# Optimization experiments

Measured on AMD Instinct MI355X. Metric: run time of the kernel, lower is better.

## Reference

```python
import jax, jax.numpy as jnp
import numpy as np

DIM = 384
WS = 7
NH = 12
N = WS ** 3          # 343 tokens per window
BW = 256             # number of windows (batch*num_windows)
HD = DIM // NH       # head dim = 32


def _rel_pos_index(ws: int) -> np.ndarray:
    coords = np.stack(np.meshgrid(np.arange(ws), np.arange(ws), np.arange(ws), indexing='ij'))
    coords = coords.reshape(3, -1)                       # [3, N]
    rel = coords[:, :, None] - coords[:, None, :]        # [3, N, N]
    rel = rel.transpose(1, 2, 0)                         # [N, N, 3]
    rel = rel + (ws - 1)
    idx = rel[..., 0] * (2 * ws - 1) ** 2 + rel[..., 1] * (2 * ws - 1) + rel[..., 2]
    return idx.astype(np.int32)                          # [N, N]


def setup_inputs() -> dict:
    key = jax.random.key(0)
    ks = jax.random.split(key, 6)
    x = jax.random.normal(ks[0], (BW, N, DIM), dtype=jnp.float32)
    qkv_w = jax.random.normal(ks[1], (DIM, 3 * DIM), dtype=jnp.float32) * (DIM ** -0.5)
    qkv_b = jax.random.normal(ks[2], (3 * DIM,), dtype=jnp.float32) * 0.02
    proj_w = jax.random.normal(ks[3], (DIM, DIM), dtype=jnp.float32) * (DIM ** -0.5)
    proj_b = jax.random.normal(ks[4], (DIM,), dtype=jnp.float32) * 0.02
    bias_table = jax.random.normal(ks[5], ((2 * WS - 1) ** 3, NH), dtype=jnp.float32) * 0.02
    rel_pos_index = jnp.asarray(_rel_pos_index(WS))
    return {"x": x, "qkv_w": qkv_w, "qkv_b": qkv_b, "proj_w": proj_w,
            "proj_b": proj_b, "bias_table": bias_table, "rel_pos_index": rel_pos_index}


def reference(x, qkv_w, qkv_b, proj_w, proj_b, bias_table, rel_pos_index):
    B_, n, C = x.shape
    scale = (C // NH) ** -0.5
    qkv = (x @ qkv_w + qkv_b).reshape(B_, n, 3, NH, C // NH)
    q, k, v = qkv[:, :, 0], qkv[:, :, 1], qkv[:, :, 2]   # [B_, n, H, d]
    # scores: [B_, H, n, n]
    attn = jnp.einsum('bihd,bjhd->bhij', q, k) * scale
    rel_bias = bias_table[rel_pos_index]                  # [n, n, H]
    attn = attn + rel_bias.transpose(2, 0, 1)[None]
    attn = jax.nn.softmax(attn, axis=-1)
    out = jnp.einsum('bhij,bjhd->bihd', attn, v).reshape(B_, n, C)
    return out @ proj_w + proj_b
```

## Files before the change

kernel.cpp:

```cpp
#include <hip/hip_runtime.h>


#define M_TOT 87808
#define NTOK  343
#define DIMC  384
#define NHEAD 12
#define QKVN  1152
#define BWIN  256
#define TSLAB (22 * 11 * 512)

typedef __bf16 bf16x8 __attribute__((ext_vector_type(8)));
typedef __bf16 bf16x4 __attribute__((ext_vector_type(4)));
typedef float f32x4 __attribute__((ext_vector_type(4)));
typedef unsigned short u16x4 __attribute__((ext_vector_type(4)));
typedef unsigned short u16x8 __attribute__((ext_vector_type(8)));

__device__ __forceinline__ unsigned short bf16rne(float f) {
  unsigned int u = __float_as_uint(f);
  u += 0x7fffu + ((u >> 16) & 1u);
  return (unsigned short)(u >> 16);
}

__device__ __forceinline__ unsigned int packbf(float lo, float hi) {
  return (unsigned int)bf16rne(lo) | ((unsigned int)bf16rne(hi) << 16);
}

__device__ __forceinline__ bf16x4 pack_bf16x4(float a, float b, float c, float d) {
  unsigned ua = __float_as_uint(a) + 0x8000u;
  unsigned ub = __float_as_uint(b) + 0x8000u;
  unsigned uc = __float_as_uint(c) + 0x8000u;
  unsigned ud = __float_as_uint(d) + 0x8000u;
  unsigned lo = __builtin_amdgcn_perm(ub, ua, 0x07060302u);
  unsigned hi = __builtin_amdgcn_perm(ud, uc, 0x07060302u);
  union { unsigned u[2]; bf16x4 v; } x;
  x.u[0] = lo; x.u[1] = hi;
  return x.v;
}

__device__ __forceinline__ float bf16tof(unsigned short s) {
  return __uint_as_float(((unsigned int)s) << 16);
}

__device__ __forceinline__ u16x4 lo4(u16x8 v) { return __builtin_shufflevector(v, v, 0, 1, 2, 3); }
__device__ __forceinline__ u16x4 hi4(u16x8 v) { return __builtin_shufflevector(v, v, 4, 5, 6, 7); }


__global__ void cvt_x_kernel(const float* __restrict__ x, unsigned short* __restrict__ xb, int n8) {
  int i = blockIdx.x * 256 + threadIdx.x;
  if (i >= n8) return;
  const float4* xv = (const float4*)x + (size_t)i * 2;
  float4 a = xv[0], b = xv[1];
  uint4 o;
  o.x = packbf(a.x, a.y); o.y = packbf(a.z, a.w);
  o.z = packbf(b.x, b.y); o.w = packbf(b.z, b.w);
  ((uint4*)xb)[i] = o;
}

__global__ void prep_w_kernel(const float* __restrict__ qkv_w, const float* __restrict__ proj_w,
                              unsigned short* __restrict__ wqkvT, unsigned short* __restrict__ wprojT) {
  int tid = blockIdx.x * 256 + threadIdx.x;
  if (tid < QKVN * DIMC) {
    int n = tid / DIMC, k = tid - n * DIMC;
    wqkvT[tid] = bf16rne(qkv_w[(size_t)k * QKVN + n]);
  }
  if (tid < DIMC * DIMC) {
    int n = tid / DIMC, k = tid - n * DIMC;
    wprojT[tid] = bf16rne(proj_w[(size_t)k * DIMC + n]);
  }
}

__global__ void prep_biasT_kernel(const float* __restrict__ bias_table, const int* __restrict__ rel_idx,
                                  unsigned short* __restrict__ biasT) {
  int tid = blockIdx.x * 256 + threadIdx.x;
  if (tid >= NHEAD * 22 * 11 * 64) return;
  int l15 = tid & 15;
  int q   = (tid >> 4) & 3;
  int rest = tid >> 6;
  int jp  = rest % 11;
  int it  = (rest / 11) % 22;
  int h   = rest / (11 * 22);
  int i = it * 16 + l15; if (i > NTOK - 1) i = NTOK - 1;
  const float LOG2E = 1.44269504088896340f;
  u16x8 out;
  #pragma unroll
  for (int e = 0; e < 8; e++) {
    int jt = 2 * jp + (e >> 2), r = e & 3;
    int j = jt * 16 + 4 * q + r;
    float v;
    if (j < NTOK) {
      int idx = rel_idx[i * NTOK + j];
      v = bias_table[idx * NHEAD + h] * LOG2E;
    } else {
      v = -1e30f;
    }
    out[e] = bf16rne(v);
  }
  *(u16x8*)(biasT + (size_t)tid * 8) = out;
}


typedef const __attribute__((address_space(1))) unsigned int* gas_t;
typedef __attribute__((address_space(3))) unsigned int* las_t;

__device__ __forceinline__ void load16_lds(const void* g, void* l) {
  __builtin_amdgcn_global_load_lds((gas_t)g, (las_t)l, 16, 0, 0);
}

template<int OUT_MODE>
__global__ __launch_bounds__(256, 3) void gemm_bt_kernel(
    const unsigned short* __restrict__ A, const unsigned short* __restrict__ Bt,
    const float* __restrict__ bias, void* __restrict__ outp,
    int M, int Nn, int K)
{
  __shared__ __attribute__((aligned(16))) unsigned short Atile[128 * 64];
  __shared__ __attribute__((aligned(16))) unsigned short Btile[128 * 64];
  const int t = threadIdx.x;
  const int lane = t & 63, w = t >> 6;
  const int q = lane >> 4, l15 = lane & 15;
  const int m0 = blockIdx.y * 128, n0 = blockIdx.x * 128;
  const int wm = w >> 1, wn = w & 1;

  f32x4 acc[4][4] = {};

  for (int kk = 0; kk < K; kk += 64) {
    #pragma unroll
    for (int i = 0; i < 4; i++) {
      int chunk = i * 256 + t;
      int r = chunk >> 3, cl = chunk & 7;
      int cg = cl ^ (r & 7);
      load16_lds(A + (size_t)(m0 + r) * K + kk + cg * 8, Atile + chunk * 8);
      load16_lds(Bt + (size_t)(n0 + r) * K + kk + cg * 8, Btile + chunk * 8);
    }
    __syncthreads();
    const bf16x8* As = (const bf16x8*)Atile;
    const bf16x8* Bs = (const bf16x8*)Btile;
    #pragma unroll
    for (int kq = 0; kq < 2; kq++) {
      bf16x8 af[4], bfr[4];
      #pragma unroll
      for (int mt = 0; mt < 4; mt++) {
        int m = wm * 64 + mt * 16 + l15;
        af[mt] = As[m * 8 + ((kq * 4 + q) ^ (m & 7))];
      }
      #pragma unroll
      for (int nt = 0; nt < 4; nt++) {
        int nr = wn * 64 + nt * 16 + l15;
        bfr[nt] = Bs[nr * 8 + ((kq * 4 + q) ^ (nr & 7))];
      }
      #pragma unroll
      for (int mt = 0; mt < 4; mt++)
        #pragma unroll
        for (int nt = 0; nt < 4; nt++)
          acc[mt][nt] = __builtin_amdgcn_mfma_f32_16x16x32_bf16(af[mt], bfr[nt], acc[mt][nt], 0, 0, 0);
    }
    __syncthreads();
  }

  #pragma unroll
  for (int nt = 0; nt < 4; nt++) {
    int nn = n0 + wn * 64 + nt * 16;
    float bv = bias[nn + l15];
    #pragma unroll
    for (int mt = 0; mt < 4; mt++) {
      int mb = m0 + wm * 64 + mt * 16 + q * 4;
      #pragma unroll
      for (int r = 0; r < 4; r++) {
        float v = acc[mt][nt][r] + bv;
        if (OUT_MODE == 0) {
          ((float*)outp)[(size_t)(mb + r) * Nn + nn + l15] = v;
        } else {
          int which = nn / DIMC;
          int hh = (nn - which * DIMC) >> 5;
          int d0 = nn & 16;
          size_t off = ((size_t)(which * NHEAD + hh) * M_TOT + (mb + r)) * 32 + d0 + l15;
          ((unsigned short*)outp)[off] = bf16rne(v);
        }
      }
    }
  }
}


#define VST 360

__global__ __launch_bounds__(512, 4) void attn_kernel(
    const unsigned short* __restrict__ qhead,
    const unsigned short* __restrict__ biasT,
    unsigned short* __restrict__ attnout)
{
  __shared__ __attribute__((aligned(16))) unsigned short Klds[22 * 512];
  __shared__ __attribute__((aligned(16))) unsigned short Vt[32 * VST];
  const int bx = blockIdx.x;
  const int g = bx & 7, s = bx >> 3;
  int h, b;
  if (s < 256) { h = g; b = s; }
  else { int j = g * 128 + (s - 256); h = 8 + (j >> 8); b = j & 255; }

  const int t = threadIdx.x;
  const int lane = t & 63, w = t >> 6;
  const int q = lane >> 4, l15 = lane & 15;

  const unsigned short* Qslab = qhead + ((size_t)(0 * NHEAD + h) * M_TOT + (size_t)b * NTOK) * 32;
  const unsigned short* Kslab = qhead + ((size_t)(1 * NHEAD + h) * M_TOT + (size_t)b * NTOK) * 32;
  const unsigned short* Vslab = qhead + ((size_t)(2 * NHEAD + h) * M_TOT + (size_t)b * NTOK) * 32;

  for (int jt = w; jt < 22; jt += 8)
    load16_lds(Kslab + (size_t)(jt * 16 + l15) * 32 + q * 8, Klds + jt * 512 + lane * 8);

  for (int j = t; j < NTOK; j += 512) {
    #pragma unroll
    for (int c = 0; c < 4; c++) {
      uint4 vd = *(const uint4*)(Vslab + (size_t)j * 32 + c * 8);
      const unsigned short* vs = (const unsigned short*)&vd;
      #pragma unroll
      for (int u = 0; u < 8; u++)
        Vt[(c * 8 + u) * VST + j] = vs[u];
    }
  }
  for (int idx = t; idx < 32 * 16; idx += 512)
    Vt[(idx >> 4) * VST + NTOK + (idx & 15)] = 0;
  __syncthreads();

  const float CS = 0.17677669529663689f * 1.44269504088896340f;

  for (int pr = w; pr < 11; pr += 8) {
    int i0 = pr * 32;
    int iqA = i0 + l15;      iqA = iqA > (NTOK - 1) ? (NTOK - 1) : iqA;
    int iqB = i0 + 16 + l15; iqB = iqB > (NTOK - 1) ? (NTOK - 1) : iqB;
    bf16x8 bqA = *(const bf16x8*)(Qslab + (size_t)iqA * 32 + q * 8);
    bf16x8 bqB = *(const bf16x8*)(Qslab + (size_t)iqB * 32 + q * 8);

    const unsigned short* bApt = biasT + ((size_t)(h * 22 + pr * 2) * 11) * 512 + q * 128 + l15 * 8;
    const unsigned short* bBpt = bApt + 11 * 512;

    f32x4 oA0 = {0.f,0.f,0.f,0.f}, oA1 = {0.f,0.f,0.f,0.f};
    f32x4 oB0 = {0.f,0.f,0.f,0.f}, oB1 = {0.f,0.f,0.f,0.f};
    float denA = 0.f, denB = 0.f;

    auto jt_step = [&](int jt, u16x4 cbA, u16x4 cbB) {
      bf16x8 ak = *(const bf16x8*)(Klds + jt * 512 + lane * 8);
      f32x4 z = {0.f,0.f,0.f,0.f};
      f32x4 sA = __builtin_amdgcn_mfma_f32_16x16x32_bf16(ak, bqA, z, 0, 0, 0);
      f32x4 sB = __builtin_amdgcn_mfma_f32_16x16x32_bf16(ak, bqB, z, 0, 0, 0);
      float pA0 = __builtin_amdgcn_exp2f(fmaf(sA[0], CS, bf16tof(cbA[0])));
      float pA1 = __builtin_amdgcn_exp2f(fmaf(sA[1], CS, bf16tof(cbA[1])));
      float pA2 = __builtin_amdgcn_exp2f(fmaf(sA[2], CS, bf16tof(cbA[2])));
      float pA3 = __builtin_amdgcn_exp2f(fmaf(sA[3], CS, bf16tof(cbA[3])));
      float pB0 = __builtin_amdgcn_exp2f(fmaf(sB[0], CS, bf16tof(cbB[0])));
      float pB1 = __builtin_amdgcn_exp2f(fmaf(sB[1], CS, bf16tof(cbB[1])));
      float pB2 = __builtin_amdgcn_exp2f(fmaf(sB[2], CS, bf16tof(cbB[2])));
      float pB3 = __builtin_amdgcn_exp2f(fmaf(sB[3], CS, bf16tof(cbB[3])));
      denA += (pA0 + pA1) + (pA2 + pA3);
      denB += (pB0 + pB1) + (pB2 + pB3);
      bf16x4 pfA = pack_bf16x4(pA0, pA1, pA2, pA3);
      bf16x4 pfB = pack_bf16x4(pB0, pB1, pB2, pB3);
      bf16x4 vf0 = *(const bf16x4*)(Vt + l15 * VST + jt * 16 + 4 * q);
      bf16x4 vf1 = *(const bf16x4*)(Vt + (16 + l15) * VST + jt * 16 + 4 * q);
      oA0 = __builtin_amdgcn_mfma_f32_16x16x16bf16_1k(pfA, vf0, oA0, 0, 0, 0);
      oA1 = __builtin_amdgcn_mfma_f32_16x16x16bf16_1k(pfA, vf1, oA1, 0, 0, 0);
      oB0 = __builtin_amdgcn_mfma_f32_16x16x16bf16_1k(pfB, vf0, oB0, 0, 0, 0);
      oB1 = __builtin_amdgcn_mfma_f32_16x16x16bf16_1k(pfB, vf1, oB1, 0, 0, 0);
    };

    u16x8 bufX_A = *(const u16x8*)(bApt);
    u16x8 bufX_B = *(const u16x8*)(bBpt);
    u16x8 bufY_A = *(const u16x8*)(bApt + 512);
    u16x8 bufY_B = *(const u16x8*)(bBpt + 512);

    for (int jp = 0; jp < 10; jp += 2) {
      jt_step(2 * jp,     lo4(bufX_A), lo4(bufX_B));
      jt_step(2 * jp + 1, hi4(bufX_A), hi4(bufX_B));
      bufX_A = *(const u16x8*)(bApt + (jp + 2) * 512);
      bufX_B = *(const u16x8*)(bBpt + (jp + 2) * 512);
      jt_step(2 * jp + 2, lo4(bufY_A), lo4(bufY_B));
      jt_step(2 * jp + 3, hi4(bufY_A), hi4(bufY_B));
      int c3 = (jp + 3 > 10) ? 10 : (jp + 3);
      bufY_A = *(const u16x8*)(bApt + c3 * 512);
      bufY_B = *(const u16x8*)(bBpt + c3 * 512);
    }
    jt_step(20, lo4(bufX_A), lo4(bufX_B));
    jt_step(21, hi4(bufX_A), hi4(bufX_B));

    denA += __shfl_xor(denA, 16); denA += __shfl_xor(denA, 32);
    denB += __shfl_xor(denB, 16); denB += __shfl_xor(denB, 32);

    #pragma unroll
    for (int r = 0; r < 4; r++) {
      int rr = 4 * q + r;
      float dA = __shfl(denA, rr);
      float dB = __shfl(denB, rr);
      int iA = i0 + rr, iB = i0 + 16 + rr;
      if (iA < NTOK) {
        float inv = __builtin_amdgcn_rcpf(dA);
        size_t orow = ((size_t)b * NTOK + iA) * DIMC + h * 32;
        attnout[orow + l15]      = bf16rne(oA0[r] * inv);
        attnout[orow + 16 + l15] = bf16rne(oA1[r] * inv);
      }
      if (iB < NTOK) {
        float inv = __builtin_amdgcn_rcpf(dB);
        size_t orow = ((size_t)b * NTOK + iB) * DIMC + h * 32;
        attnout[orow + l15]      = bf16rne(oB0[r] * inv);
        attnout[orow + 16 + l15] = bf16rne(oB1[r] * inv);
      }
    }
  }
}


extern "C" void kernel_launch(void* const* d_in, const int* in_sizes, int n_in,
                              void* d_out, int out_size, void* d_ws, size_t ws_size,
                              hipStream_t stream) {
  const float* x          = (const float*)d_in[0];
  const float* qkv_w      = (const float*)d_in[1];
  const float* qkv_b      = (const float*)d_in[2];
  const float* proj_w     = (const float*)d_in[3];
  const float* proj_b     = (const float*)d_in[4];
  const float* bias_table = (const float*)d_in[5];
  const int*   rel_idx    = (const int*)d_in[6];

  char* p = (char*)d_ws;
  unsigned short* xb      = (unsigned short*)p; p += (size_t)M_TOT * DIMC * 2;
  unsigned short* wqkvT   = (unsigned short*)p; p += (size_t)QKVN * DIMC * 2;
  unsigned short* wprojT  = (unsigned short*)p; p += (size_t)DIMC * DIMC * 2;
  unsigned short* biasT   = (unsigned short*)p; p += (size_t)NHEAD * TSLAB * 2;
  unsigned short* qhead   = (unsigned short*)p; p += (size_t)3 * NHEAD * M_TOT * 32 * 2;
  unsigned short* attnout = (unsigned short*)p; p += (size_t)M_TOT * DIMC * 2;

  cvt_x_kernel<<<(M_TOT * DIMC / 8 + 255) / 256, 256, 0, stream>>>(x, xb, M_TOT * DIMC / 8);
  prep_w_kernel<<<(QKVN * DIMC + 255) / 256, 256, 0, stream>>>(qkv_w, proj_w, wqkvT, wprojT);
  prep_biasT_kernel<<<(NHEAD * 22 * 11 * 64 + 255) / 256, 256, 0, stream>>>(bias_table, rel_idx, biasT);
  gemm_bt_kernel<1><<<dim3(QKVN / 128, M_TOT / 128), 256, 0, stream>>>(
      xb, wqkvT, qkv_b, (void*)qhead, M_TOT, QKVN, DIMC);
  attn_kernel<<<BWIN * NHEAD, 512, 0, stream>>>(qhead, biasT, attnout);
  gemm_bt_kernel<0><<<dim3(DIMC / 128, M_TOT / 128), 256, 0, stream>>>(
      attnout, wprojT, proj_b, d_out, M_TOT, DIMC, DIMC);
}
```

Baseline: 577.4 us.

## Compute softmax denominator via MFMA with ones and use fp32 bias, one tile per wave

The attention kernel now computes the softmax row sums with an extra MFMA against a ones vector instead of scalar adds plus cross-lane shuffles. Each wave handles one 16-row query tile instead of a pair of tiles. The relative-position bias table is stored as fp32 rather than bf16, which removes the unpack step but doubles the bias bytes loaded per tile. Using one tile per wave lowers register pressure, but each wave now issues fewer MFMAs, so K and V fragments are reused across less work.

New measurement: 875.6 us. 51.6% more time.

```diff
diff --git a/kernel.cpp b/kernel.cpp
--- a/kernel.cpp
+++ b/kernel.cpp
@@ -12,8 +12,6 @@
 typedef __bf16 bf16x8 __attribute__((ext_vector_type(8)));
 typedef __bf16 bf16x4 __attribute__((ext_vector_type(4)));
 typedef float f32x4 __attribute__((ext_vector_type(4)));
-typedef unsigned short u16x4 __attribute__((ext_vector_type(4)));
-typedef unsigned short u16x8 __attribute__((ext_vector_type(8)));
 
 __device__ __forceinline__ unsigned short bf16rne(float f) {
   unsigned int u = __float_as_uint(f);
@@ -37,13 +35,6 @@
   return x.v;
 }
 
-__device__ __forceinline__ float bf16tof(unsigned short s) {
-  return __uint_as_float(((unsigned int)s) << 16);
-}
-
-__device__ __forceinline__ u16x4 lo4(u16x8 v) { return __builtin_shufflevector(v, v, 0, 1, 2, 3); }
-__device__ __forceinline__ u16x4 hi4(u16x8 v) { return __builtin_shufflevector(v, v, 4, 5, 6, 7); }
-
 
 __global__ void cvt_x_kernel(const float* __restrict__ x, unsigned short* __restrict__ xb, int n8) {
   int i = blockIdx.x * 256 + threadIdx.x;
@@ -70,7 +61,7 @@
 }
 
 __global__ void prep_biasT_kernel(const float* __restrict__ bias_table, const int* __restrict__ rel_idx,
-                                  unsigned short* __restrict__ biasT) {
+                                  float* __restrict__ biasT) {
   int tid = blockIdx.x * 256 + threadIdx.x;
   if (tid >= NHEAD * 22 * 11 * 64) return;
   int l15 = tid & 15;
@@ -81,21 +72,21 @@
   int h   = rest / (11 * 22);
   int i = it * 16 + l15; if (i > NTOK - 1) i = NTOK - 1;
   const float LOG2E = 1.44269504088896340f;
-  u16x8 out;
+  float o[8];
   #pragma unroll
   for (int e = 0; e < 8; e++) {
     int jt = 2 * jp + (e >> 2), r = e & 3;
     int j = jt * 16 + 4 * q + r;
-    float v;
     if (j < NTOK) {
       int idx = rel_idx[i * NTOK + j];
-      v = bias_table[idx * NHEAD + h] * LOG2E;
+      o[e] = bias_table[idx * NHEAD + h] * LOG2E;
     } else {
-      v = -1e30f;
-    }
-    out[e] = bf16rne(v);
-  }
-  *(u16x8*)(biasT + (size_t)tid * 8) = out;
+      o[e] = -1e30f;
+    }
+  }
+  float4* dst = (float4*)(biasT + (size_t)tid * 8);
+  dst[0] = make_float4(o[0], o[1], o[2], o[3]);
+  dst[1] = make_float4(o[4], o[5], o[6], o[7]);
 }
 
 
@@ -185,7 +176,7 @@
 
 __global__ __launch_bounds__(512, 4) void attn_kernel(
     const unsigned short* __restrict__ qhead,
-    const unsigned short* __restrict__ biasT,
+    const float* __restrict__ biasT,
     unsigned short* __restrict__ attnout)
 {
   __shared__ __attribute__((aligned(16))) unsigned short Klds[22 * 512];
@@ -223,84 +214,63 @@
 
   const float CS = 0.17677669529663689f * 1.44269504088896340f;
 
-  for (int pr = w; pr < 11; pr += 8) {
-    int i0 = pr * 32;
-    int iqA = i0 + l15;      iqA = iqA > (NTOK - 1) ? (NTOK - 1) : iqA;
-    int iqB = i0 + 16 + l15; iqB = iqB > (NTOK - 1) ? (NTOK - 1) : iqB;
-    bf16x8 bqA = *(const bf16x8*)(Qslab + (size_t)iqA * 32 + q * 8);
-    bf16x8 bqB = *(const bf16x8*)(Qslab + (size_t)iqB * 32 + q * 8);
-
-    const unsigned short* bApt = biasT + ((size_t)(h * 22 + pr * 2) * 11) * 512 + q * 128 + l15 * 8;
-    const unsigned short* bBpt = bApt + 11 * 512;
-
-    f32x4 oA0 = {0.f,0.f,0.f,0.f}, oA1 = {0.f,0.f,0.f,0.f};
-    f32x4 oB0 = {0.f,0.f,0.f,0.f}, oB1 = {0.f,0.f,0.f,0.f};
-    float denA = 0.f, denB = 0.f;
-
-    auto jt_step = [&](int jt, u16x4 cbA, u16x4 cbB) {
+  union { unsigned u[2]; bf16x4 v; } ones_u;
+  ones_u.u[0] = 0x3F803F80u; ones_u.u[1] = 0x3F803F80u;
+  const bf16x4 ones4 = ones_u.v;
+
+  for (int it = w; it < 22; it += 8) {
+    int i0 = it * 16;
+    int iq = i0 + l15; iq = iq > (NTOK - 1) ? (NTOK - 1) : iq;
+    bf16x8 bq = *(const bf16x8*)(Qslab + (size_t)iq * 32 + q * 8);
+
+    const float* bpt = biasT + ((size_t)(h * 22 + it) * 11) * 512 + q * 128 + l15 * 8;
+
+    f32x4 o0 = {0.f,0.f,0.f,0.f}, o1 = {0.f,0.f,0.f,0.f};
+    f32x4 den = {0.f,0.f,0.f,0.f};
+
+    auto jt_step = [&](int jt, f32x4 cb) {
       bf16x8 ak = *(const bf16x8*)(Klds + jt * 512 + lane * 8);
       f32x4 z = {0.f,0.f,0.f,0.f};
-      f32x4 sA = __builtin_amdgcn_mfma_f32_16x16x32_bf16(ak, bqA, z, 0, 0, 0);
-      f32x4 sB = __builtin_amdgcn_mfma_f32_16x16x32_bf16(ak, bqB, z, 0, 0, 0);
-      float pA0 = __builtin_amdgcn_exp2f(fmaf(sA[0], CS, bf16tof(cbA[0])));
-      float pA1 = __builtin_amdgcn_exp2f(fmaf(sA[1], CS, bf16tof(cbA[1])));
-      float pA2 = __builtin_amdgcn_exp2f(fmaf(sA[2], CS, bf16tof(cbA[2])));
-      float pA3 = __builtin_amdgcn_exp2f(fmaf(sA[3], CS, bf16tof(cbA[3])));
-      float pB0 = __builtin_amdgcn_exp2f(fmaf(sB[0], CS, bf16tof(cbB[0])));
-      float pB1 = __builtin_amdgcn_exp2f(fmaf(sB[1], CS, bf16tof(cbB[1])));
-      float pB2 = __builtin_amdgcn_exp2f(fmaf(sB[2], CS, bf16tof(cbB[2])));
-      float pB3 = __builtin_amdgcn_exp2f(fmaf(sB[3], CS, bf16tof(cbB[3])));
-      denA += (pA0 + pA1) + (pA2 + pA3);
-      denB += (pB0 + pB1) + (pB2 + pB3);
-      bf16x4 pfA = pack_bf16x4(pA0, pA1, pA2, pA3);
-      bf16x4 pfB = pack_bf16x4(pB0, pB1, pB2, pB3);
+      f32x4 sS = __builtin_amdgcn_mfma_f32_16x16x32_bf16(ak, bq, z, 0, 0, 0);
+      float p0 = __builtin_amdgcn_exp2f(fmaf(sS[0], CS, cb[0]));
+      float p1 = __builtin_amdgcn_exp2f(fmaf(sS[1], CS, cb[1]));
+      float p2 = __builtin_amdgcn_exp2f(fmaf(sS[2], CS, cb[2]));
+      float p3 = __builtin_amdgcn_exp2f(fmaf(sS[3], CS, cb[3]));
+      bf16x4 pf = pack_bf16x4(p0, p1, p2, p3);
       bf16x4 vf0 = *(const bf16x4*)(Vt + l15 * VST + jt * 16 + 4 * q);
       bf16x4 vf1 = *(const bf16x4*)(Vt + (16 + l15) * VST + jt * 16 + 4 * q);
-      oA0 = __builtin_amdgcn_mfma_f32_16x16x16bf16_1k(pfA, vf0, oA0, 0, 0, 0);
-      oA1 = __builtin_amdgcn_mfma_f32_16x16x16bf16_1k(pfA, vf1, oA1, 0, 0, 0);
-      oB0 = __builtin_amdgcn_mfma_f32_16x16x16bf16_1k(pfB, vf0, oB0, 0, 0, 0);
-      oB1 = __builtin_amdgcn_mfma_f32_16x16x16bf16_1k(pfB, vf1, oB1, 0, 0, 0);
+      den = __builtin_amdgcn_mfma_f32_16x16x16bf16_1k(pf, ones4, den, 0, 0, 0);
+      o0  = __builtin_amdgcn_mfma_f32_16x16x16bf16_1k(pf, vf0, o0, 0, 0, 0);
+      o1  = __builtin_amdgcn_mfma_f32_16x16x16bf16_1k(pf, vf1, o1, 0, 0, 0);
     };
 
-    u16x8 bufX_A = *(const u16x8*)(bApt);
-    u16x8 bufX_B = *(const u16x8*)(bBpt);
-    u16x8 bufY_A = *(const u16x8*)(bApt + 512);
-    u16x8 bufY_B = *(const u16x8*)(bBpt + 512);
+    f32x4 bX0 = *(const f32x4*)(bpt);
+    f32x4 bX1 = *(const f32x4*)(bpt + 4);
+    f32x4 bY0 = *(const f32x4*)(bpt + 512);
+    f32x4 bY1 = *(const f32x4*)(bpt + 516);
 
     for (int jp = 0; jp < 10; jp += 2) {
-      jt_step(2 * jp,     lo4(bufX_A), lo4(bufX_B));
-      jt_step(2 * jp + 1, hi4(bufX_A), hi4(bufX_B));
-      bufX_A = *(const u16x8*)(bApt + (jp + 2) * 512);
-      bufX_B = *(const u16x8*)(bBpt + (jp + 2) * 512);
-      jt_step(2 * jp + 2, lo4(bufY_A), lo4(bufY_B));
-      jt_step(2 * jp + 3, hi4(bufY_A), hi4(bufY_B));
+      jt_step(2 * jp,     bX0);
+      jt_step(2 * jp + 1, bX1);
+      bX0 = *(const f32x4*)(bpt + (jp + 2) * 512);
+      bX1 = *(const f32x4*)(bpt + (jp + 2) * 512 + 4);
+      jt_step(2 * jp + 2, bY0);
+      jt_step(2 * jp + 3, bY1);
       int c3 = (jp + 3 > 10) ? 10 : (jp + 3);
-      bufY_A = *(const u16x8*)(bApt + c3 * 512);
-      bufY_B = *(const u16x8*)(bBpt + c3 * 512);
-    }
-    jt_step(20, lo4(bufX_A), lo4(bufX_B));
-    jt_step(21, hi4(bufX_A), hi4(bufX_B));
-
-    denA += __shfl_xor(denA, 16); denA += __shfl_xor(denA, 32);
-    denB += __shfl_xor(denB, 16); denB += __shfl_xor(denB, 32);
+      bY0 = *(const f32x4*)(bpt + c3 * 512);
+      bY1 = *(const f32x4*)(bpt + c3 * 512 + 4);
+    }
+    jt_step(20, bX0);
+    jt_step(21, bX1);
 
     #pragma unroll
     for (int r = 0; r < 4; r++) {
-      int rr = 4 * q + r;
-      float dA = __shfl(denA, rr);
-      float dB = __shfl(denB, rr);
-      int iA = i0 + rr, iB = i0 + 16 + rr;
-      if (iA < NTOK) {
-        float inv = __builtin_amdgcn_rcpf(dA);
-        size_t orow = ((size_t)b * NTOK + iA) * DIMC + h * 32;
-        attnout[orow + l15]      = bf16rne(oA0[r] * inv);
-        attnout[orow + 16 + l15] = bf16rne(oA1[r] * inv);
-      }
-      if (iB < NTOK) {
-        float inv = __builtin_amdgcn_rcpf(dB);
-        size_t orow = ((size_t)b * NTOK + iB) * DIMC + h * 32;
-        attnout[orow + l15]      = bf16rne(oB0[r] * inv);
-        attnout[orow + 16 + l15] = bf16rne(oB1[r] * inv);
+      int row = i0 + 4 * q + r;
+      if (row < NTOK) {
+        float inv = __builtin_amdgcn_rcpf(den[r]);
+        size_t orow = ((size_t)b * NTOK + row) * DIMC + h * 32;
+        attnout[orow + l15]      = bf16rne(o0[r] * inv);
+        attnout[orow + 16 + l15] = bf16rne(o1[r] * inv);
       }
     }
   }
@@ -322,7 +292,7 @@
   unsigned short* xb      = (unsigned short*)p; p += (size_t)M_TOT * DIMC * 2;
   unsigned short* wqkvT   = (unsigned short*)p; p += (size_t)QKVN * DIMC * 2;
   unsigned short* wprojT  = (unsigned short*)p; p += (size_t)DIMC * DIMC * 2;
-  unsigned short* biasT   = (unsigned short*)p; p += (size_t)NHEAD * TSLAB * 2;
+  float*          biasT   = (float*)p;          p += (size_t)NHEAD * TSLAB * 4;
   unsigned short* qhead   = (unsigned short*)p; p += (size_t)3 * NHEAD * M_TOT * 32 * 2;
   unsigned short* attnout = (unsigned short*)p; p += (size_t)M_TOT * DIMC * 2;
 
```
